# Performance work log

Hardware: AMD Instinct MI355X
Metric: run time of the kernel (lower is better)

## Reference

```python
import jax, jax.numpy as jnp
import numpy as np

B, S0, S1 = 4, 768, 256
T = S0 + S1
W0, W1 = 2048, 1024
N, K, H = 8, 1, 256  # num_heads, num_kv_heads (MQA), head_dim
G = N // K
MAX_WAVELENGTH = 10000.0
BIG_NEG = -2.3819763e+38


def _apply_rope(x, positions):
    """RoPE: positions [B,L] applied to x [B,L,heads,H]."""
    half = x.shape[-1] // 2
    freq_exponents = (2.0 / x.shape[-1]) * jnp.arange(half, dtype=jnp.float32)
    timescale = MAX_WAVELENGTH ** freq_exponents  # [half]
    radians = positions[..., None].astype(jnp.float32) / timescale  # [B,L,half]
    radians = radians[..., None, :]  # [B,L,1,half]
    sin, cos = jnp.sin(radians), jnp.cos(radians)
    x1, x2 = jnp.split(x.astype(jnp.float32), 2, axis=-1)
    res = jnp.concatenate([x1 * cos - x2 * sin, x2 * cos + x1 * sin], axis=-1)
    return res.astype(x.dtype)


def setup_inputs() -> dict:
    key = jax.random.key(0)
    ks = jax.random.split(key, 8)
    x0 = jax.random.normal(ks[0], (B, S0, W0), dtype=jnp.float32)
    x1 = jax.random.normal(ks[1], (B, S1, W1), dtype=jnp.float32)
    positions = jnp.broadcast_to(jnp.arange(T, dtype=jnp.int32)[None, :], (B, T))
    # causal mask [B,1,T,T]
    attn_mask = jnp.broadcast_to(jnp.tril(jnp.ones((T, T), dtype=bool))[None, None], (B, 1, T, T))
    # lecun_normal on the width (in) axis
    q0_w = jax.random.normal(ks[2], (N, W0, H), dtype=jnp.float32) / np.sqrt(W0)
    kv0_w = jax.random.normal(ks[3], (2, K, W0, H), dtype=jnp.float32) / np.sqrt(W0)
    out0_w = jax.random.normal(ks[4], (N, H, W0), dtype=jnp.float32) / np.sqrt(N * H)
    q1_w = jax.random.normal(ks[5], (N, W1, H), dtype=jnp.float32) / np.sqrt(W1)
    kv1_w = jax.random.normal(ks[6], (2, K, W1, H), dtype=jnp.float32) / np.sqrt(W1)
    out1_w = jax.random.normal(ks[7], (N, H, W1), dtype=jnp.float32) / np.sqrt(N * H)
    return {"x0": x0, "x1": x1, "positions": positions, "attn_mask": attn_mask,
            "q0_w": q0_w, "kv0_w": kv0_w, "out0_w": out0_w,
            "q1_w": q1_w, "kv1_w": kv1_w, "out1_w": out1_w}


def reference(x0, x1, positions, attn_mask, q0_w, kv0_w, out0_w, q1_w, kv1_w, out1_w):
    dtype = x0.dtype
    # per-modality QKV projections (num_kv_heads != num_heads branch)
    q0 = jnp.einsum('BTD,NDH->BTNH', x0, q0_w.astype(dtype))
    k0, v0 = jnp.einsum('BSD,2KDH->2BSKH', x0, kv0_w.astype(dtype))
    q1 = jnp.einsum('BTD,NDH->BTNH', x1, q1_w.astype(dtype))
    k1, v1 = jnp.einsum('BSD,2KDH->2BSKH', x1, kv1_w.astype(dtype))
    q = jnp.concatenate([q0, q1], axis=1)  # [B,T,N,H]
    k = jnp.concatenate([k0, k1], axis=1)  # [B,T,K,H]
    v = jnp.concatenate([v0, v1], axis=1)
    q = _apply_rope(q, positions) * (H ** -0.5)
    k = _apply_rope(k, positions)
    # prefill cache init: cache_size == attn_mask.shape[-1] == T, so no padding
    idx = jnp.full((B,), T, dtype=jnp.int32)
    # GQA attention
    qg = q.reshape(B, T, K, G, H)  # 'B T (K G) H -> B T K G H'
    logits = jnp.einsum('BTKGH,BSKH->BKGTS', qg, k, preferred_element_type=jnp.float32)
    masked = jnp.where(attn_mask[:, :, None, :, :], logits, BIG_NEG)
    probs = jax.nn.softmax(masked, axis=-1).astype(dtype)
    enc = jnp.einsum('BKGTS,BSKH->BTKGH', probs, v).reshape(B, T, N, H)
    out0 = jnp.einsum('BTNH,NHD->BTD', enc[:, :S0], out0_w.astype(dtype))
    out1 = jnp.einsum('BTNH,NHD->BTD', enc[:, S0:], out1_w.astype(dtype))
    return (out0, out1, idx, k, v)
```

## Files before the change

kernel.cpp:

```cpp
#include <hip/hip_runtime.h>

typedef unsigned short u16;
typedef __attribute__((ext_vector_type(8))) short short8;
typedef __attribute__((ext_vector_type(4))) float f32x4;
typedef __attribute__((ext_vector_type(4))) unsigned short u16x4;

__device__ __forceinline__ u16 f2bf(float f){
  unsigned u = __float_as_uint(f);
  u += 0x7FFFu + ((u >> 16) & 1u);
  return (u16)(u >> 16);
}
__device__ __forceinline__ float bf2f(u16 h){
  return __uint_as_float(((unsigned)h) << 16);
}
__device__ __forceinline__ void gload16(const void* g, void* l){
  __builtin_amdgcn_global_load_lds((const __attribute__((address_space(1))) void*)g,
                                   (__attribute__((address_space(3))) void*)l, 16, 0, 0);
}
__device__ __forceinline__ f32x4 mfma16(short8 a, short8 b, f32x4 c){
  return __builtin_amdgcn_mfma_f32_16x16x32_bf16(a, b, c, 0, 0, 0);
}
__device__ __forceinline__ short8 ld8(const u16* p){
  return *reinterpret_cast<const short8*>(p);
}
__device__ __forceinline__ unsigned cvtpk(float lo, float hi){
  unsigned r;
  asm volatile("v_cvt_pk_bf16_f32 %0, %1, %2" : "=v"(r) : "v"(lo), "v"(hi));
  return r;
}

__device__ __forceinline__
void transp_body(const float* __restrict__ S, u16* __restrict__ D,
                 int K, int C, int kb, int cb){
  __shared__ float t[32][33];
  int tx = threadIdx.x & 31, ty = threadIdx.x >> 5;
  #pragma unroll
  for (int i = ty; i < 32; i += 8)
    t[i][tx] = S[(size_t)(kb + i) * C + cb + tx];
  __syncthreads();
  #pragma unroll
  for (int i = ty; i < 32; i += 8)
    D[(size_t)(cb + i) * K + kb + tx] = f2bf(t[tx][i]);
}
__global__ __launch_bounds__(256)
void prep_all(const float* __restrict__ x0, const float* __restrict__ x1,
              u16* __restrict__ x0b, u16* __restrict__ x1b,
              const float* q0_w, const float* kv0_w, const float* q1_w,
              const float* kv1_w, const float* o0_w, const float* o1_w,
              u16* qkv0T, u16* qkv1T, u16* o0T, u16* o1T){
  int bid = blockIdx.x;
  if (bid < 7168){
    const float* s; u16* d; int i;
    if (bid < 6144){ s = x0; d = x0b; i = bid * 256 + threadIdx.x; }
    else           { s = x1; d = x1b; i = (bid - 6144) * 256 + threadIdx.x; }
    float4 v = reinterpret_cast<const float4*>(s)[i];
    u16x4 o = { f2bf(v.x), f2bf(v.y), f2bf(v.z), f2bf(v.w) };
    reinterpret_cast<u16x4*>(d)[i] = o;
    return;
  }
  bid -= 7168;
  const float* S; u16* D; int K, C, nkc, lid;
  if (bid < 4096){
    S = q0_w; D = qkv0T; K = 2048; C = 256; lid = bid;
  } else if (bid < 5120){
    S = kv0_w; D = qkv0T + (size_t)2048*2048; K = 2048; C = 256; lid = bid - 4096;
  } else if (bid < 7168){
    S = q1_w; D = qkv1T; K = 1024; C = 256; lid = bid - 5120;
  } else if (bid < 7680){
    S = kv1_w; D = qkv1T + (size_t)2048*1024; K = 1024; C = 256; lid = bid - 7168;
  } else if (bid < 11776){
    S = o0_w; D = o0T; K = 2048; C = 2048; lid = bid - 7680;
  } else {
    S = o1_w; D = o1T; K = 2048; C = 1024; lid = bid - 11776;
  }
  nkc = (K >> 5) * (C >> 5);
  int z   = lid / nkc;
  int rem = lid - z * nkc;
  int kb  = (rem / (C >> 5)) << 5;
  int cb  = (rem % (C >> 5)) << 5;
  transp_body(S + (size_t)z * K * C, D + (size_t)z * K * C, K, C, kb, cb);
}

__device__ __forceinline__
void gemm_body(const u16* __restrict__ A, int lda, int aS, int aT, int aOff,
               const u16* __restrict__ BT, int ldbt,
               u16* __restrict__ Cb, float* __restrict__ Cf, int ldc,
               int cS, int cT, int cOff, int N, int Kd, int bid, char* smem){
  int ntx = N >> 7;
  int bm = bid / ntx;
  int bn = bid - bm * ntx;
  int row0 = bm << 7, col0 = bn << 7;
  size_t arow0 = (size_t)(row0 / aS) * aT + (row0 % aS) + aOff;
  size_t crow0 = (size_t)(row0 / cS) * cT + (row0 % cS) + cOff;
  const u16* Abase = A + arow0 * (size_t)lda;
  const u16* Bbase = BT + (size_t)col0 * ldbt;
  int tid = threadIdx.x;
  int w = tid >> 6, l = tid & 63;
  int wr = (w >> 1) << 6, wc = (w & 1) << 6;
  int lr = l & 15, g4 = l >> 4, lq = (l >> 4) << 2;
  int keyr = lr & 7;
  f32x4 acc[4][4];
  #pragma unroll
  for (int m = 0; m < 4; m++)
    #pragma unroll
    for (int n = 0; n < 4; n++)
      acc[m][n] = (f32x4){0.f, 0.f, 0.f, 0.f};
  int scol = (((tid & 7) ^ ((tid >> 3) & 7)) << 3);
  const u16* gA = Abase + (size_t)(tid >> 3) * lda + scol;
  const u16* gB = Bbase + (size_t)(tid >> 3) * ldbt + scol;
  int dsto = tid * 16;

  auto STAGE = [&](char* dst, int k0){
    gload16(gA + k0,                      dst + dsto);
    gload16(gA + (size_t)32*lda  + k0,    dst + 4096  + dsto);
    gload16(gA + (size_t)64*lda  + k0,    dst + 8192  + dsto);
    gload16(gA + (size_t)96*lda  + k0,    dst + 12288 + dsto);
    gload16(gB + k0,                      dst + 16384 + dsto);
    gload16(gB + (size_t)32*ldbt + k0,    dst + 20480 + dsto);
    gload16(gB + (size_t)64*ldbt + k0,    dst + 24576 + dsto);
    gload16(gB + (size_t)96*ldbt + k0,    dst + 28672 + dsto);
  };

  STAGE(smem, 0);
  int cur = 0;
  for (int k0 = 0; k0 < Kd; k0 += 64, cur ^= 1){
    asm volatile("s_waitcnt vmcnt(0)" ::: "memory");
    __builtin_amdgcn_s_barrier();
    asm volatile("" ::: "memory");
    if (k0 + 64 < Kd)
      STAGE(smem + (cur ^ 1) * 32768, k0 + 64);
    const u16* As = (const u16*)(smem + cur * 32768);
    const u16* Bs = As + 8192;
    #pragma unroll
    for (int kk = 0; kk < 2; kk++){
      int so = ((g4 + kk*4) ^ keyr) << 3;
      short8 af[4], bfr[4];
      #pragma unroll
      for (int m = 0; m < 4; m++)
        af[m] = ld8(&As[(wr + m*16 + lr)*64 + so]);
      #pragma unroll
      for (int n = 0; n < 4; n++)
        bfr[n] = ld8(&Bs[(wc + n*16 + lr)*64 + so]);
      #pragma unroll
      for (int m = 0; m < 4; m++)
        #pragma unroll
        for (int n = 0; n < 4; n++)
          acc[m][n] = mfma16(af[m], bfr[n], acc[m][n]);
    }
  }
  #pragma unroll
  for (int m = 0; m < 4; m++){
    #pragma unroll
    for (int i = 0; i < 4; i++){
      size_t r = crow0 + wr + m*16 + lq + i;
      if (Cb){
        #pragma unroll
        for (int n = 0; n < 4; n++)
          Cb[r*ldc + col0 + wc + n*16 + lr] = f2bf(acc[m][n][i]);
      } else {
        #pragma unroll
        for (int n = 0; n < 4; n++)
          Cf[r*ldc + col0 + wc + n*16 + lr] = acc[m][n][i];
      }
    }
  }
}

__global__ __launch_bounds__(256)
void gemm_qkv(const u16* __restrict__ x0b, const u16* __restrict__ qkv0T,
              const u16* __restrict__ x1b, const u16* __restrict__ qkv1T,
              u16* __restrict__ qkvb){
  extern __shared__ __align__(16) char smem[];
  int bid = blockIdx.x;
  if (bid < 480)
    gemm_body(x0b, 2048, 3072, 3072, 0, qkv0T, 2048,
              qkvb, nullptr, 2560, 768, 1024, 0, 2560, 2048, bid, smem);
  else
    gemm_body(x1b, 1024, 1024, 1024, 0, qkv1T, 1024,
              qkvb, nullptr, 2560, 256, 1024, 768, 2560, 1024, bid - 480, smem);
}

__global__ __launch_bounds__(256)
void gemm_out(const u16* __restrict__ encb, const u16* __restrict__ o0T,
              const u16* __restrict__ o1T, float* __restrict__ out0,
              float* __restrict__ out1){
  extern __shared__ __align__(16) char smem[];
  int bid = blockIdx.x;
  if (bid < 384)
    gemm_body(encb, 2048, 768, 1024, 0, o0T, 2048,
              nullptr, out0, 2048, 3072, 3072, 0, 2048, 2048, bid, smem);
  else
    gemm_body(encb, 2048, 256, 1024, 768, o1T, 2048,
              nullptr, out1, 1024, 1024, 1024, 0, 1024, 2048, bid - 384, smem);
}

__global__ __launch_bounds__(256)
void rope_tv(u16* __restrict__ qkv, const int* __restrict__ positions,
             float* __restrict__ k_out, float* __restrict__ v_out,
             float* __restrict__ idx_out, u16* __restrict__ vT){
  int bid = blockIdx.x;
  int tid = threadIdx.x;
  if (bid < 2048){
    int bt = bid*2 + (tid >> 7);
    int j = tid & 127;
    float pos = (float)positions[bt];
    float ts = powf(10000.0f, (float)j * 0.0078125f);
    float rad = pos / ts;
    float sn, cs;
    sincosf(rad, &sn, &cs);
    u16* q = qkv + (size_t)bt * 2560;
    #pragma unroll
    for (int n = 0; n < 8; n++){
      float x1 = bf2f(q[n*256 + j]);
      float x2 = bf2f(q[n*256 + 128 + j]);
      q[n*256 + j]       = f2bf((x1*cs - x2*sn) * 0.0625f);
      q[n*256 + 128 + j] = f2bf((x2*cs + x1*sn) * 0.0625f);
    }
    u16* kv = q + 2048;
    float x1 = bf2f(kv[j]), x2 = bf2f(kv[128 + j]);
    float k1 = x1*cs - x2*sn, k2 = x2*cs + x1*sn;
    kv[j] = f2bf(k1); kv[128 + j] = f2bf(k2);
    size_t ko = (size_t)bt * 256;
    k_out[ko + j] = k1;  k_out[ko + 128 + j] = k2;
    v_out[ko + j] = bf2f(kv[256 + j]);
    v_out[ko + 128 + j] = bf2f(kv[384 + j]);
    if (bt == 0 && j < 4 && tid < 128) idx_out[j] = 1024.0f;
    return;
  }
  __shared__ u16 t[32][33];
  int lid = bid - 2048;
  int b = lid >> 8;
  int rem = lid & 255;
  int tb = (rem >> 3) << 5;
  int hb = (rem & 7) << 5;
  int tx = tid & 31, ty = tid >> 5;
  #pragma unroll
  for (int i = ty; i < 32; i += 8)
    t[i][tx] = qkv[(size_t)(b*1024 + tb + i)*2560 + 2304 + hb + tx];
  __syncthreads();
  #pragma unroll
  for (int i = ty; i < 32; i += 8)
    vT[(size_t)(b*256 + hb + i)*1024 + tb + tx] = t[tx][i];
}

__global__ __launch_bounds__(256, 2)
void attn_kernel(const u16* __restrict__ qkv, const u16* __restrict__ vT,
                 u16* __restrict__ enc){
  extern __shared__ __align__(16) char smem[];
  int bid = blockIdx.x;
  int b   = bid & 3;
  int h2  = (bid >> 2) & 1;
  int idx = (bid >> 3) & 31;
  int qt  = (bid < 256) ? (63 - idx) : idx;
  int tid = threadIdx.x;
  int w = tid >> 6;
  int head = h2*4 + w;
  int l = tid & 63;
  int lr = l & 15;
  int g = l >> 4;
  int lkqe  = g << 3;
  int lkq16 = g << 4;
  int q0 = qt << 4, nkv = q0 + 16;
  int swk = (lr & 7) << 4;
  int swv = ((lr >> 1) & 3) << 4;

  const char* kbase = (const char*)qkv + (size_t)b*5242880 + 4096;
  const char* vbase = (const char*)vT + (size_t)b*524288;
  const char* ksrc[4]; const char* vsrc[4];
  int kldo[4], vldo[4];
  #pragma unroll
  for (int r = 0; r < 4; r++){
    int o = r*4096 + tid*16;
    int krow = o >> 9;
    int kcol = (o & 511) ^ ((krow & 7) << 4);
    ksrc[r] = kbase + (size_t)krow*5120 + kcol;
    kldo[r] = o;
    int vrow = o >> 6;
    int vcol = (o & 63) ^ (((vrow >> 1) & 3) << 4);
    vsrc[r] = vbase + (size_t)vrow*2048 + vcol;
    vldo[r] = 16384 + o;
  }

  const u16* qb = qkv + ((size_t)(b*1024 + q0)) * 2560 + head*256;
  short8 qf[8];
  #pragma unroll
  for (int hf = 0; hf < 8; hf++)
    qf[hf] = ld8(qb + (size_t)lr*2560 + hf*32 + lkqe);

  f32x4 o_[16];
  #pragma unroll
  for (int hf = 0; hf < 16; hf++)
    o_[hf] = (f32x4){0.f,0.f,0.f,0.f};
  float mrow = -3.0e38f, lrow = 0.f;

  auto STAGE = [&](int buf, int kt){
    char* dst = smem + buf*32768;
    #pragma unroll
    for (int r = 0; r < 4; r++)
      gload16(ksrc[r] + (size_t)kt*5120, dst + kldo[r]);
    #pragma unroll
    for (int r = 0; r < 4; r++)
      gload16(vsrc[r] + (size_t)kt*2, dst + vldo[r]);
  };

  STAGE(0, 0);
  int cur = 0;
  for (int kt = 0; kt < nkv; kt += 32, cur ^= 1){
    asm volatile("s_waitcnt vmcnt(0)" ::: "memory");
    __builtin_amdgcn_s_barrier();
    asm volatile("" ::: "memory");
    if (kt + 32 < nkv)
      STAGE(cur ^ 1, kt + 32);

    const char* Kb = smem + cur*32768;
    const char* Vb = Kb + 16384;
    f32x4 s[2];
    s[0] = (f32x4){0.f,0.f,0.f,0.f};
    s[1] = (f32x4){0.f,0.f,0.f,0.f};
    __builtin_amdgcn_s_setprio(1);
    #pragma unroll
    for (int hf = 0; hf < 8; hf++){
      int colb = (hf*64 + lkq16) ^ swk;
      short8 k0 = *(const short8*)(Kb + (size_t)(lr     )*512 + colb);
      short8 k1 = *(const short8*)(Kb + (size_t)(lr + 16)*512 + colb);
      s[0] = mfma16(k0, qf[hf], s[0]);
      s[1] = mfma16(k1, qf[hf], s[1]);
    }
    __builtin_amdgcn_s_setprio(0);
    if (kt + 32 > q0){
      #pragma unroll
      for (int cf = 0; cf < 2; cf++)
        #pragma unroll
        for (int i = 0; i < 4; i++){
          int kv_g = kt + cf*16 + g*4 + i;
          if (kv_g > q0 + lr) s[cf][i] = -1.0e30f;
        }
    }
    float lm = fmaxf(fmaxf(fmaxf(s[0][0], s[0][1]), fmaxf(s[0][2], s[0][3])),
                     fmaxf(fmaxf(s[1][0], s[1][1]), fmaxf(s[1][2], s[1][3])));
    if (__ballot(lm > mrow + 8.f)){
      float m8 = fmaxf(lm, __shfl_xor(lm, 16, 64));
      m8 = fmaxf(m8, __shfl_xor(m8, 32, 64));
      float mn = fmaxf(mrow, m8);
      float corr = __expf(mrow - mn);
      mrow = mn;
      lrow *= corr;
      #pragma unroll
      for (int hf = 0; hf < 16; hf++)
        #pragma unroll
        for (int i = 0; i < 4; i++)
          o_[hf][i] *= corr;
    }
    float p[2][4];
    #pragma unroll
    for (int cf = 0; cf < 2; cf++)
      #pragma unroll
      for (int i = 0; i < 4; i++)
        p[cf][i] = __expf(s[cf][i] - mrow);
    lrow += p[0][0] + p[0][1] + p[0][2] + p[0][3]
          + p[1][0] + p[1][1] + p[1][2] + p[1][3];
    unsigned A0 = cvtpk(p[0][0], p[0][1]);
    unsigned A1 = cvtpk(p[0][2], p[0][3]);
    unsigned B0 = cvtpk(p[1][0], p[1][1]);
    unsigned B1 = cvtpk(p[1][2], p[1][3]);
    unsigned sp0 = (unsigned)__shfl_xor((int)(g < 2 ? A0 : B0), 16, 64);
    unsigned sp1 = (unsigned)__shfl_xor((int)(g < 2 ? A1 : B1), 16, 64);
    unsigned c0  = (unsigned)__shfl_xor((int)(l < 32 ? B0 : A0), 32, 64);
    unsigned c1  = (unsigned)__shfl_xor((int)(l < 32 ? B1 : A1), 32, 64);
    unsigned pc0 = (unsigned)__shfl_xor((int)c0, 16, 64);
    unsigned pc1 = (unsigned)__shfl_xor((int)c1, 16, 64);
    union { unsigned u[4]; short8 v; } pf;
    pf.u[0] = (g == 0) ? A0 : (g == 1) ? pc0 : (g == 2) ? c0  : sp0;
    pf.u[1] = (g == 0) ? A1 : (g == 1) ? pc1 : (g == 2) ? c1  : sp1;
    pf.u[2] = (g == 0) ? sp0 : (g == 1) ? c0 : (g == 2) ? pc0 : B0;
    pf.u[3] = (g == 0) ? sp1 : (g == 1) ? c1 : (g == 2) ? pc1 : B1;
    __builtin_amdgcn_s_setprio(1);
    #pragma unroll
    for (int hf = 0; hf < 16; hf++){
      const char* vr = Vb + (size_t)(hf*16 + lr)*64;
      short8 v0 = *(const short8*)(vr + (lkq16 ^ swv));
      o_[hf] = mfma16(v0, pf.v, o_[hf]);
    }
    __builtin_amdgcn_s_setprio(0);
  }
  lrow += __shfl_xor(lrow, 16, 64);
  lrow += __shfl_xor(lrow, 32, 64);
  u16* eb = enc + ((size_t)(b*1024 + q0 + lr)) * 2048 + head*256;
  float inv = 1.0f / lrow;
  #pragma unroll
  for (int hf = 0; hf < 16; hf++){
    u16x4 st = { f2bf(o_[hf][0] * inv), f2bf(o_[hf][1] * inv),
                 f2bf(o_[hf][2] * inv), f2bf(o_[hf][3] * inv) };
    *reinterpret_cast<u16x4*>(eb + hf*16 + g*4) = st;
  }
}

extern "C" void kernel_launch(void* const* d_in, const int* in_sizes, int n_in,
                              void* d_out, int out_size, void* d_ws, size_t ws_size,
                              hipStream_t stream){
  const float* x0     = (const float*)d_in[0];
  const float* x1     = (const float*)d_in[1];
  const int*   pos    = (const int*)d_in[2];
  const float* q0_w   = (const float*)d_in[4];
  const float* kv0_w  = (const float*)d_in[5];
  const float* out0_w = (const float*)d_in[6];
  const float* q1_w   = (const float*)d_in[7];
  const float* kv1_w  = (const float*)d_in[8];
  const float* out1_w = (const float*)d_in[9];

  float* out  = (float*)d_out;
  float* out0 = out;
  float* out1 = out + 6291456;
  float* idxp = out + 7340032;
  float* kout = out + 7340036;
  float* vout = out + 8388612;

  char* ws = (char*)d_ws;
  size_t off = 0;
  auto alloc = [&](size_t bytes){
    void* p = ws + off;
    off = (off + bytes + 255) & ~(size_t)255;
    return p;
  };
  u16* x0b   = (u16*)alloc((size_t)6291456 * 2);
  u16* x1b   = (u16*)alloc((size_t)1048576 * 2);
  u16* qkv0T = (u16*)alloc((size_t)2560 * 2048 * 2);
  u16* qkv1T = (u16*)alloc((size_t)2560 * 1024 * 2);
  u16* o0T   = (u16*)alloc((size_t)2048 * 2048 * 2);
  u16* o1T   = (u16*)alloc((size_t)1024 * 2048 * 2);
  u16* qkvb  = (u16*)alloc((size_t)4096 * 2560 * 2);
  u16* vTb   = (u16*)alloc((size_t)4 * 256 * 1024 * 2);
  u16* encb  = (u16*)alloc((size_t)4096 * 2048 * 2);

  hipFuncSetAttribute((const void*)attn_kernel,
                      hipFuncAttributeMaxDynamicSharedMemorySize, 65536);
  hipFuncSetAttribute((const void*)gemm_qkv,
                      hipFuncAttributeMaxDynamicSharedMemorySize, 65536);
  hipFuncSetAttribute((const void*)gemm_out,
                      hipFuncAttributeMaxDynamicSharedMemorySize, 65536);

  prep_all<<<20992, 256, 0, stream>>>(x0, x1, x0b, x1b,
                                      q0_w, kv0_w, q1_w, kv1_w, out0_w, out1_w,
                                      qkv0T, qkv1T, o0T, o1T);

  gemm_qkv<<<640, 256, 65536, stream>>>(x0b, qkv0T, x1b, qkv1T, qkvb);

  rope_tv<<<3072, 256, 0, stream>>>(qkvb, pos, kout, vout, idxp, vTb);

  attn_kernel<<<512, 256, 65536, stream>>>(qkvb, vTb, encb);

  gemm_out<<<448, 256, 65536, stream>>>(encb, o0T, o1T, out0, out1);
}
```

Baseline: 152.0 us.

## Move output-weight transposes into QKV GEMM launch to fill idle CUs

Output projection weight transposes are removed from the prep kernel and appended as extra blocks of the QKV GEMM launch. They are intended to overlap with the GEMM's partial last wave and shorten the prep kernel. The transpose blocks now inherit the GEMM's 64KB dynamic LDS allocation, which limits how many can be resident per CU.

Result: slower. 160.0 us (+5.3%).

```diff
diff --git a/kernel.cpp b/kernel.cpp
--- a/kernel.cpp
+++ b/kernel.cpp
@@ -31,8 +31,8 @@
 
 __device__ __forceinline__
 void transp_body(const float* __restrict__ S, u16* __restrict__ D,
-                 int K, int C, int kb, int cb){
-  __shared__ float t[32][33];
+                 int K, int C, int kb, int cb, char* smem){
+  float (*t)[33] = (float (*)[33])smem;
   int tx = threadIdx.x & 31, ty = threadIdx.x >> 5;
   #pragma unroll
   for (int i = ty; i < 32; i += 8)
@@ -42,12 +42,13 @@
   for (int i = ty; i < 32; i += 8)
     D[(size_t)(cb + i) * K + kb + tx] = f2bf(t[tx][i]);
 }
+
 __global__ __launch_bounds__(256)
 void prep_all(const float* __restrict__ x0, const float* __restrict__ x1,
               u16* __restrict__ x0b, u16* __restrict__ x1b,
               const float* q0_w, const float* kv0_w, const float* q1_w,
-              const float* kv1_w, const float* o0_w, const float* o1_w,
-              u16* qkv0T, u16* qkv1T, u16* o0T, u16* o1T){
+              const float* kv1_w, u16* qkv0T, u16* qkv1T){
+  __shared__ __align__(16) char smem[4352];
   int bid = blockIdx.x;
   if (bid < 7168){
     const float* s; u16* d; int i;
@@ -66,19 +67,15 @@
     S = kv0_w; D = qkv0T + (size_t)2048*2048; K = 2048; C = 256; lid = bid - 4096;
   } else if (bid < 7168){
     S = q1_w; D = qkv1T; K = 1024; C = 256; lid = bid - 5120;
-  } else if (bid < 7680){
+  } else {
     S = kv1_w; D = qkv1T + (size_t)2048*1024; K = 1024; C = 256; lid = bid - 7168;
-  } else if (bid < 11776){
-    S = o0_w; D = o0T; K = 2048; C = 2048; lid = bid - 7680;
-  } else {
-    S = o1_w; D = o1T; K = 2048; C = 1024; lid = bid - 11776;
   }
   nkc = (K >> 5) * (C >> 5);
   int z   = lid / nkc;
   int rem = lid - z * nkc;
   int kb  = (rem / (C >> 5)) << 5;
   int cb  = (rem % (C >> 5)) << 5;
-  transp_body(S + (size_t)z * K * C, D + (size_t)z * K * C, K, C, kb, cb);
+  transp_body(S + (size_t)z * K * C, D + (size_t)z * K * C, K, C, kb, cb, smem);
 }
 
 __device__ __forceinline__
@@ -169,15 +166,28 @@
 __global__ __launch_bounds__(256)
 void gemm_qkv(const u16* __restrict__ x0b, const u16* __restrict__ qkv0T,
               const u16* __restrict__ x1b, const u16* __restrict__ qkv1T,
-              u16* __restrict__ qkvb){
+              u16* __restrict__ qkvb,
+              const float* __restrict__ o0_w, const float* __restrict__ o1_w,
+              u16* __restrict__ o0T, u16* __restrict__ o1T){
   extern __shared__ __align__(16) char smem[];
   int bid = blockIdx.x;
-  if (bid < 480)
+  if (bid < 480){
     gemm_body(x0b, 2048, 3072, 3072, 0, qkv0T, 2048,
               qkvb, nullptr, 2560, 768, 1024, 0, 2560, 2048, bid, smem);
-  else
+    return;
+  }
+  if (bid < 640){
     gemm_body(x1b, 1024, 1024, 1024, 0, qkv1T, 1024,
               qkvb, nullptr, 2560, 256, 1024, 768, 2560, 1024, bid - 480, smem);
+    return;
+  }
+  int lid = bid - 640;
+  const float* S; u16* D; int K, C;
+  if (lid < 4096){ S = o0_w; D = o0T; K = 2048; C = 2048; }
+  else           { S = o1_w; D = o1T; K = 2048; C = 1024; lid -= 4096; }
+  int kb = (lid / (C >> 5)) << 5;
+  int cb = (lid % (C >> 5)) << 5;
+  transp_body(S, D, K, C, kb, cb, smem);
 }
 
 __global__ __launch_bounds__(256)
@@ -439,11 +449,11 @@
   hipFuncSetAttribute((const void*)gemm_out,
                       hipFuncAttributeMaxDynamicSharedMemorySize, 65536);
 
-  prep_all<<<20992, 256, 0, stream>>>(x0, x1, x0b, x1b,
-                                      q0_w, kv0_w, q1_w, kv1_w, out0_w, out1_w,
-                                      qkv0T, qkv1T, o0T, o1T);
-
-  gemm_qkv<<<640, 256, 65536, stream>>>(x0b, qkv0T, x1b, qkv1T, qkvb);
+  prep_all<<<14848, 256, 0, stream>>>(x0, x1, x0b, x1b,
+                                      q0_w, kv0_w, q1_w, kv1_w, qkv0T, qkv1T);
+
+  gemm_qkv<<<6784, 256, 65536, stream>>>(x0b, qkv0T, x1b, qkv1T, qkvb,
+                                         out0_w, out1_w, o0T, o1T);
 
   rope_tv<<<3072, 256, 0, stream>>>(qkvb, pos, kout, vout, idxp, vTb);
 
```
